# Kernel optimization log

Hardware: AMD Instinct MI355X
Metric: run time of the kernel (lower is better)

Reference implementation:

```python
import jax, jax.numpy as jnp
import numpy as np

N = 100000      # nodes
R = 4           # relations
E = 500000      # edges per relation
IN, HID, OUT = 256, 128, 64


def _graphconv(x, src, dst, W, b, n_nodes):
    """DGL GraphConv, norm='both': D_dst^{-1/2} A (D_src^{-1/2} x) W + b.
    Transform-first (in_feats >= out_feats path); math identical either way."""
    e = src.shape[0]
    ones = jnp.ones((e,), x.dtype)
    deg_out = jnp.clip(jax.ops.segment_sum(ones, src, num_segments=n_nodes), 1.0)
    deg_in = jnp.clip(jax.ops.segment_sum(ones, dst, num_segments=n_nodes), 1.0)
    h = (x * jax.lax.rsqrt(deg_out)[:, None]) @ W           # [N, out]
    agg = jax.ops.segment_sum(h[src], dst, num_segments=n_nodes)  # scatter-add over edges
    return agg * jax.lax.rsqrt(deg_in)[:, None] + b


def _hetero_layer(x, edges_src, edges_dst, W, b, n_nodes):
    # HeteroGraphConv(aggregate='sum'): sum of per-relation GraphConv outputs
    out = _graphconv(x, edges_src[0], edges_dst[0], W[0], b[0], n_nodes)
    for r in range(1, W.shape[0]):
        out = out + _graphconv(x, edges_src[r], edges_dst[r], W[r], b[r], n_nodes)
    return out


def setup_inputs() -> dict:
    key = jax.random.key(0)
    ks = jax.random.split(key, 8)
    x = jax.random.normal(ks[0], (N, IN), dtype=jnp.float32)
    edges_src = jax.random.randint(ks[1], (R, E), 0, N, dtype=jnp.int32)
    edges_dst = jax.random.randint(ks[2], (R, E), 0, N, dtype=jnp.int32)
    s1 = 1.0 / np.sqrt(IN)
    s2 = 1.0 / np.sqrt(HID)
    W1 = jax.random.uniform(ks[3], (R, IN, HID), jnp.float32, -s1, s1)
    b1 = jnp.zeros((R, HID), jnp.float32)
    W2 = jax.random.uniform(ks[4], (R, HID, OUT), jnp.float32, -s2, s2)
    b2 = jnp.zeros((R, OUT), jnp.float32)
    return {"x": x, "edges_src": edges_src, "edges_dst": edges_dst,
            "W1": W1, "b1": b1, "W2": W2, "b2": b2}


def reference(x, edges_src, edges_dst, W1, b1, W2, b2):
    h = _hetero_layer(x, edges_src, edges_dst, W1, b1, N)
    h = jax.nn.relu(h)
    out = _hetero_layer(h, edges_src, edges_dst, W2, b2, N)
    return out
```

## Files before the change

### kernel.cpp

```cpp
#include <hip/hip_runtime.h>

#define NN   100000
#define RR   4
#define EE   500000
#define FIN  256
#define FHID 128
#define FOUT 64
#define NBLK ((NN + 255) / 256)
#define NPAD (NN + 32)
#define NSHARD 8

#define PEDGE  ((RR * EE + 255) / 256)
#define PCW1   (RR * FIN * FHID / 256)
#define PCW2   (RR * FHID * FOUT / 256)
#define CONVW_GRID (PCW1 + PCW2 + 1)

#define NG1    ((NN + 127) / 128 * 4)
#define K1_PER 1564
#define K1_GRID (7 * K1_PER)

typedef unsigned short u16;
typedef unsigned char  u8;
typedef unsigned int   u32;
typedef __attribute__((ext_vector_type(8))) __bf16 bf16x8;
typedef __attribute__((ext_vector_type(4))) float  f32x4;
typedef __attribute__((ext_vector_type(4))) u32    u32x4;

__device__ __forceinline__ u16 f2bf(float f) {
    union { float f; u32 u; } v; v.f = f;
    u32 r = v.u + 0x7FFFu + ((v.u >> 16) & 1u);
    return (u16)(r >> 16);
}
__device__ __forceinline__ u32 pack2bf(float x, float y) {
    return ((u32)f2bf(y) << 16) | (u32)f2bf(x);
}

__device__ __forceinline__ float2 bfx2(u32 v) {
    union { u32 u; float f; } a, b;
    a.u = v << 16; b.u = v & 0xFFFF0000u;
    return {a.f, b.f};
}

typedef __attribute__((address_space(3))) u32 lds_u32;
typedef __attribute__((address_space(1))) const u32 gl_u32;
__device__ __forceinline__ void gload16(const void* g, void* l) {
    __builtin_amdgcn_global_load_lds((gl_u32*)g, (lds_u32*)l, 16, 0, 0);
}

__global__ __launch_bounds__(256) void convw_kernel(
        const float* __restrict__ W1, u16* __restrict__ W1t,
        const float* __restrict__ W2, u16* __restrict__ W2t,
        const float* __restrict__ b1, const float* __restrict__ b2,
        float* __restrict__ sb1, float* __restrict__ sb2) {
    int bx = blockIdx.x, t = threadIdx.x;
    if (bx < PCW1) {
        int i = bx * 256 + t;
        int r = i / (FIN * FHID);
        int rem = i - r * FIN * FHID;
        int k = rem / FHID, n = rem - k * FHID;
        W1t[((size_t)r * FHID + n) * FIN + k] = f2bf(W1[i]);
    } else if (bx < PCW1 + PCW2) {
        int i = (bx - PCW1) * 256 + t;
        int r = i / (FHID * FOUT);
        int rem = i - r * FHID * FOUT;
        int k = rem / FOUT, n = rem - k * FOUT;
        W2t[((size_t)r * FOUT + n) * FHID + k] = f2bf(W2[i]);
    } else {
        if (t < FHID) {
            float v = 0.f;
            for (int r = 0; r < RR; ++r) v += b1[r * FHID + t];
            sb1[t] = v;
        } else if (t < FHID + FOUT) {
            int j = t - FHID;
            float v = 0.f;
            for (int r = 0; r < RR; ++r) v += b2[r * FOUT + j];
            sb2[j] = v;
        }
    }
}

__device__ __forceinline__ void gemm1_body(u16* As, u16* Bs,
                                           const float* __restrict__ X,
                                           const u16* __restrict__ Bt,
                                           u16* __restrict__ Y, int M,
                                           int m0, int n0) {
    int tid = threadIdx.x;
    int wave = tid >> 6, lane = tid & 63;
    int quad = lane >> 4, l15 = lane & 15;
    int wm = (wave >> 1) * 64, wn = (wave & 1) * 64;

    int arow = tid >> 1;
    int acol = (tid & 1) * 16;
    const float4* Ag = (const float4*)(X + (size_t)min(m0 + arow, M - 1) * FIN + acol);
    u32* Aw = (u32*)As + arow * 16 + (acol >> 1);

    int srow = tid >> 2;
    int scol = (tid & 3) * 8;
    const u16* Bg0 = Bt + (size_t)(n0 + srow) * FIN + scol;
    const u16* Bg1 = Bt + (size_t)(n0 + srow + 64) * FIN + scol;
    u16* Bs0 = Bs + tid * 8;
    u16* Bs1 = Bs + 2048 + tid * 8;

    const bf16x8* Ard = (const bf16x8*)(As + (wm + l15) * 32 + quad * 8);
    const bf16x8* Brd = (const bf16x8*)(Bs + (wn + l15) * 32 + quad * 8);

    f32x4 acc[4][4] = {};
    for (int k0 = 0; k0 < FIN; k0 += 32) {
        gload16(Bg0 + k0, Bs0);
        gload16(Bg1 + k0, Bs1);
        float4 f0 = Ag[(k0 >> 2) + 0], f1 = Ag[(k0 >> 2) + 1];
        float4 f2 = Ag[(k0 >> 2) + 2], f3 = Ag[(k0 >> 2) + 3];
        u32x4 w0 = {pack2bf(f0.x, f0.y), pack2bf(f0.z, f0.w),
                    pack2bf(f1.x, f1.y), pack2bf(f1.z, f1.w)};
        u32x4 w1 = {pack2bf(f2.x, f2.y), pack2bf(f2.z, f2.w),
                    pack2bf(f3.x, f3.y), pack2bf(f3.z, f3.w)};
        ((u32x4*)Aw)[0] = w0;
        ((u32x4*)Aw)[1] = w1;
        __syncthreads();
        bf16x8 af[4], bfr[4];
#pragma unroll
        for (int i = 0; i < 4; ++i) af[i]  = Ard[i * 64];
#pragma unroll
        for (int j = 0; j < 4; ++j) bfr[j] = Brd[j * 64];
#pragma unroll
        for (int i = 0; i < 4; ++i)
#pragma unroll
            for (int j = 0; j < 4; ++j)
                acc[i][j] = __builtin_amdgcn_mfma_f32_16x16x32_bf16(af[i], bfr[j], acc[i][j], 0, 0, 0);
        __syncthreads();
    }

#pragma unroll
    for (int i = 0; i < 4; ++i) {
#pragma unroll
        for (int r = 0; r < 4; ++r) {
            int row = m0 + wm + i * 16 + quad * 4 + r;
            if (row < M) {
#pragma unroll
                for (int j = 0; j < 4; ++j) {
                    int col = n0 + wn + j * 16 + l15;
                    Y[(size_t)row * (RR * FHID) + col] = f2bf(acc[i][j][r]);
                }
            }
        }
    }
}

__global__ __launch_bounds__(256) void count_gemm(
        const float* __restrict__ x, const u16* __restrict__ W1t,
        u16* __restrict__ Y,
        const int* __restrict__ esrc, const int* __restrict__ edst,
        u32* __restrict__ cnt2,
        u8* __restrict__ pos8) {
    __shared__ u16 As[128 * 32];
    __shared__ u16 Bs[128 * 32];
    int p = blockIdx.x / 7, q = blockIdx.x - p * 7;
    if (q < 2) {
        int gb = p * 2 + q;
        if (gb >= NG1) return;
        gemm1_body(As, Bs, x, W1t, Y, NN, (gb >> 2) * 128, (gb & 3) * 128);
    } else {
        int i = (p * 5 + (q - 2)) * 256 + threadIdx.x;
        if (i >= RR * EE) return;
        u32* co = cnt2 + (size_t)(blockIdx.x & (NSHARD - 1)) * 2 * NPAD;
        int r = i / EE;
        int s = esrc[i], d = edst[i];
        atomicAdd(&co[s], 1u << (8 * r));
        u32 old = atomicAdd(&co[NPAD + d], 1u << (8 * r));
        pos8[i] = (u8)((old >> (8 * r)) & 255u);
    }
}

__global__ __launch_bounds__(256) void reduce_deg(const u32* __restrict__ cnt2,
                                                  f32x4* __restrict__ so,
                                                  f32x4* __restrict__ si,
                                                  u32x4* __restrict__ di4,
                                                  int* __restrict__ cnt,
                                                  int* __restrict__ bsum,
                                                  u8* __restrict__ shpre) {
    __shared__ int sh[256];
    int n = blockIdx.x * 256 + threadIdx.x;
    int c = 0;
    if (n < NN) {
        u32 osum[4] = {0, 0, 0, 0};
        u32 isum[4] = {0, 0, 0, 0};
        u32 words[8] = {0, 0, 0, 0, 0, 0, 0, 0};
#pragma unroll
        for (int s = 0; s < NSHARD; ++s) {
            u32 o = cnt2[(size_t)s * 2 * NPAD + n];
            u32 d = cnt2[(size_t)s * 2 * NPAD + NPAD + n];
#pragma unroll
            for (int k = 0; k < 4; ++k) {
                osum[k] += (o >> (8 * k)) & 255u;
                words[k * 2 + (s >> 2)] |= isum[k] << (8 * (s & 3));
                isum[k] += (d >> (8 * k)) & 255u;
            }
        }
        u32x4 dd;
        f32x4 vo, vi;
#pragma unroll
        for (int k = 0; k < 4; ++k) {
            dd[k] = isum[k];
            vo[k] = rsqrtf((float)max(osum[k], 1u));
            vi[k] = rsqrtf((float)max(isum[k], 1u));
            c += (int)isum[k];
        }
        so[n] = vo; si[n] = vi; di4[n] = dd;
        cnt[n] = c;
        u32x4* sp = (u32x4*)(shpre + (size_t)n * 32);
        u32x4 w0 = {words[0], words[1], words[2], words[3]};
        u32x4 w1 = {words[4], words[5], words[6], words[7]};
        sp[0] = w0;
        sp[1] = w1;
    }
    sh[threadIdx.x] = c;
    __syncthreads();
    for (int d = 128; d > 0; d >>= 1) {
        if (threadIdx.x < d) sh[threadIdx.x] += sh[threadIdx.x + d];
        __syncthreads();
    }
    if (threadIdx.x == 0) bsum[blockIdx.x] = sh[0];
}

__global__ __launch_bounds__(512) void scanb_kernel(const int* __restrict__ bsum,
                                                    int* __restrict__ boff) {
    __shared__ int sh[512];
    int t = threadIdx.x;
    int v = (t < NBLK) ? bsum[t] : 0;
    sh[t] = v;
    __syncthreads();
    for (int d = 1; d < 512; d <<= 1) {
        int u = (t >= d) ? sh[t - d] : 0;
        __syncthreads();
        sh[t] += u;
        __syncthreads();
    }
    if (t < NBLK) boff[t] = sh[t] - v;
}

__global__ __launch_bounds__(256) void offsets_kernel(const int* __restrict__ cnt,
                                                      const int* __restrict__ boff,
                                                      const u32x4* __restrict__ di4,
                                                      int* __restrict__ off,
                                                      u32x4* __restrict__ off4) {
    __shared__ int sh[256];
    int i = blockIdx.x * 256 + threadIdx.x;
    int t = threadIdx.x;
    int v = (i < NN) ? cnt[i] : 0;
    sh[t] = v;
    __syncthreads();
    for (int d = 1; d < 256; d <<= 1) {
        int u = (t >= d) ? sh[t - d] : 0;
        __syncthreads();
        sh[t] += u;
        __syncthreads();
    }
    int ex = boff[blockIdx.x] + sh[t] - v;
    if (i < NN) {
        off[i] = ex;
        u32x4 d = di4[i];
        u32x4 c;
        c[0] = (u32)ex;
        c[1] = c[0] + d[0];
        c[2] = c[1] + d[1];
        c[3] = c[2] + d[2];
        off4[i] = c;
    }
    if (i == NN - 1) off[NN] = ex + v;
}

__global__ __launch_bounds__(256) void place_kernel(const int* __restrict__ esrc,
                                                    const int* __restrict__ edst,
                                                    const u32* __restrict__ off4,
                                                    const u8* __restrict__ shpre,
                                                    const u8* __restrict__ pos8,
                                                    u32* __restrict__ meta) {
    int i = blockIdx.x * 256 + threadIdx.x;
    if (i >= RR * EE) return;
    int r = i / EE;
    int t = i >> 8;
    int p5 = t / 5;
    int shard = (p5 * 7 + (t - p5 * 5) + 2) & (NSHARD - 1);
    int dr = edst[i] * 4 + r;
    meta[off4[dr] + shpre[(size_t)dr * 8 + shard] + pos8[i]] = (u32)(esrc[i] * 4 + r);
}

template<int NW, int K, int LOG2F>
__global__ __launch_bounds__(256) void gemm_tile(const u16* __restrict__ A,
                                                 const u16* __restrict__ Bt,
                                                 const f32x4* __restrict__ so,
                                                 u16* __restrict__ Y, int M) {
    __shared__ u16 As[128 * 32];
    __shared__ u16 Bs[128 * 32];
    int tid = threadIdx.x;
    int m0 = blockIdx.x * 128, n0 = blockIdx.y * 128;
    int wave = tid >> 6, lane = tid & 63;
    int quad = lane >> 4, l15 = lane & 15;
    int wm = (wave >> 1) * 64, wn = (wave & 1) * 64;

    int srow = tid >> 2;
    int scol = (tid & 3) * 8;
    const u16* Ag0 = A + (size_t)min(m0 + srow,      M - 1) * K + scol;
    const u16* Ag1 = A + (size_t)min(m0 + srow + 64, M - 1) * K + scol;
    const u16* Bg0 = Bt + (size_t)(n0 + srow) * K + scol;
    const u16* Bg1 = Bt + (size_t)(n0 + srow + 64) * K + scol;
    u16* As0 = As + tid * 8;
    u16* As1 = As + 2048 + tid * 8;
    u16* Bs0 = Bs + tid * 8;
    u16* Bs1 = Bs + 2048 + tid * 8;

    const bf16x8* Ard = (const bf16x8*)(As + (wm + l15) * 32 + quad * 8);
    const bf16x8* Brd = (const bf16x8*)(Bs + (wn + l15) * 32 + quad * 8);

    f32x4 acc[4][4] = {};
    for (int k0 = 0; k0 < K; k0 += 32) {
        gload16(Ag0 + k0, As0);
        gload16(Ag1 + k0, As1);
        gload16(Bg0 + k0, Bs0);
        gload16(Bg1 + k0, Bs1);
        __syncthreads();
        bf16x8 af[4], bfr[4];
#pragma unroll
        for (int i = 0; i < 4; ++i) af[i]  = Ard[i * 64];
#pragma unroll
        for (int j = 0; j < 4; ++j) bfr[j] = Brd[j * 64];
#pragma unroll
        for (int i = 0; i < 4; ++i)
#pragma unroll
            for (int j = 0; j < 4; ++j)
                acc[i][j] = __builtin_amdgcn_mfma_f32_16x16x32_bf16(af[i], bfr[j], acc[i][j], 0, 0, 0);
        __syncthreads();
    }

#pragma unroll
    for (int i = 0; i < 4; ++i) {
#pragma unroll
        for (int r = 0; r < 4; ++r) {
            int row = m0 + wm + i * 16 + quad * 4 + r;
            if (row < M) {
                f32x4 so4 = so[row];
#pragma unroll
                for (int j = 0; j < 4; ++j) {
                    int colb = n0 + wn + j * 16;
                    float scale = so4[colb >> LOG2F];
                    Y[(size_t)row * NW + colb + l15] = f2bf(acc[i][j][r] * scale);
                }
            }
        }
    }
}


__global__ __launch_bounds__(256) void gather1(const u32* __restrict__ Y,
                                               const int* __restrict__ off,
                                               const u32* __restrict__ meta,
                                               const float* __restrict__ soF,
                                               const f32x4* __restrict__ si,
                                               const float* __restrict__ sb,
                                               u32* __restrict__ H1) {
    int wid  = blockIdx.x * 4 + (threadIdx.x >> 6);
    int lane = threadIdx.x & 63;
    if (wid >= NN) return;
    int j = off[wid], end = off[wid + 1];
    f32x4 si4 = si[wid];
    float a0x = 0.f, a0y = 0.f, a1x = 0.f, a1y = 0.f;
    float a2x = 0.f, a2y = 0.f, a3x = 0.f, a3y = 0.f;
    for (; j + 4 <= end; j += 4) {
        u32 m0 = meta[j], m1 = meta[j + 1], m2 = meta[j + 2], m3 = meta[j + 3];
        u32 v0 = Y[(size_t)m0 * 64 + lane];
        u32 v1 = Y[(size_t)m1 * 64 + lane];
        u32 v2 = Y[(size_t)m2 * 64 + lane];
        u32 v3 = Y[(size_t)m3 * 64 + lane];
        float c0 = soF[m0] * si4[m0 & 3], c1 = soF[m1] * si4[m1 & 3];
        float c2 = soF[m2] * si4[m2 & 3], c3 = soF[m3] * si4[m3 & 3];
        float2 f0 = bfx2(v0), f1 = bfx2(v1), f2 = bfx2(v2), f3 = bfx2(v3);
        a0x = fmaf(c0, f0.x, a0x); a0y = fmaf(c0, f0.y, a0y);
        a1x = fmaf(c1, f1.x, a1x); a1y = fmaf(c1, f1.y, a1y);
        a2x = fmaf(c2, f2.x, a2x); a2y = fmaf(c2, f2.y, a2y);
        a3x = fmaf(c3, f3.x, a3x); a3y = fmaf(c3, f3.y, a3y);
    }
    for (; j < end; ++j) {
        u32 m0 = meta[j];
        u32 v0 = Y[(size_t)m0 * 64 + lane];
        float2 f0 = bfx2(v0);
        float c0 = soF[m0] * si4[m0 & 3];
        a0x = fmaf(c0, f0.x, a0x); a0y = fmaf(c0, f0.y, a0y);
    }
    float2 b = ((const float2*)sb)[lane];
    float ax = fmaxf((a0x + a1x) + (a2x + a3x) + b.x, 0.f);
    float ay = fmaxf((a0y + a1y) + (a2y + a3y) + b.y, 0.f);
    H1[(size_t)wid * 64 + lane] = ((u32)f2bf(ay) << 16) | (u32)f2bf(ax);
}

__global__ __launch_bounds__(256) void gather2(const u32* __restrict__ Y,
                                               const int* __restrict__ off,
                                               const u32* __restrict__ meta,
                                               const f32x4* __restrict__ si,
                                               const float* __restrict__ sb,
                                               float* __restrict__ out) {
    int wid  = blockIdx.x * 4 + (threadIdx.x >> 6);
    int lane = threadIdx.x & 63;
    if (wid >= NN) return;
    int sub = lane >> 5, col = lane & 31;
    int end = off[wid + 1];
    int j = off[wid] + sub;
    f32x4 si4 = si[wid];
    float a0x = 0.f, a0y = 0.f, a1x = 0.f, a1y = 0.f;
    for (; j + 2 < end; j += 4) {
        u32 m0 = meta[j], m1 = meta[j + 2];
        u32 v0 = Y[(size_t)m0 * 32 + col];
        u32 v1 = Y[(size_t)m1 * 32 + col];
        float2 f0 = bfx2(v0), f1 = bfx2(v1);
        float c0 = si4[m0 & 3], c1 = si4[m1 & 3];
        a0x = fmaf(c0, f0.x, a0x); a0y = fmaf(c0, f0.y, a0y);
        a1x = fmaf(c1, f1.x, a1x); a1y = fmaf(c1, f1.y, a1y);
    }
    if (j < end) {
        u32 m0 = meta[j];
        u32 v0 = Y[(size_t)m0 * 32 + col];
        float2 f0 = bfx2(v0);
        float c0 = si4[m0 & 3];
        a0x = fmaf(c0, f0.x, a0x); a0y = fmaf(c0, f0.y, a0y);
    }
    float ax = a0x + a1x, ay = a0y + a1y;
    ax += __shfl_xor(ax, 32);
    ay += __shfl_xor(ay, 32);
    if (sub == 0) {
        float2 b = ((const float2*)sb)[col];
        float2 o = {ax + b.x, ay + b.y};
        ((float2*)out)[(size_t)wid * 32 + col] = o;
    }
}


extern "C" void kernel_launch(void* const* d_in, const int* in_sizes, int n_in,
                              void* d_out, int out_size, void* d_ws, size_t ws_size,
                              hipStream_t stream) {
    const float* x    = (const float*)d_in[0];
    const int*   esrc = (const int*)  d_in[1];
    const int*   edst = (const int*)  d_in[2];
    const float* W1   = (const float*)d_in[3];
    const float* b1   = (const float*)d_in[4];
    const float* W2   = (const float*)d_in[5];
    const float* b2   = (const float*)d_in[6];
    float* out = (float*)d_out;

    char* w = (char*)d_ws;
    auto alloc = [&](size_t bytes) -> char* {
        char* p = w; w += (bytes + 255) & ~(size_t)255; return p;
    };
    u32*   cnt2    = (u32*)  alloc((size_t)NSHARD * 2 * NPAD * 4);
    float* so      = (float*)alloc((size_t)NN * 4 * 4);
    float* si      = (float*)alloc((size_t)NN * 4 * 4);
    u32*   di4     = (u32*)  alloc((size_t)NN * 4 * 4);
    int*   cnt     = (int*)  alloc((size_t)NN * 4);
    int*   off     = (int*)  alloc((size_t)(NN + 1) * 4);
    u32*   off4    = (u32*)  alloc((size_t)NN * 4 * 4);
    int*   bsum    = (int*)  alloc((size_t)NBLK * 4);
    int*   boff    = (int*)  alloc((size_t)NBLK * 4);
    float* sb1     = (float*)alloc(FHID * 4);
    float* sb2     = (float*)alloc(FOUT * 4);
    u8*    shpre   = (u8*)   alloc((size_t)NN * 4 * NSHARD);
    u8*    pos8    = (u8*)   alloc((size_t)RR * EE);
    u16*   W1t     = (u16*)  alloc((size_t)RR * FIN * FHID * 2);
    u16*   W2t     = (u16*)  alloc((size_t)RR * FHID * FOUT * 2);
    u32*   meta    = (u32*)  alloc((size_t)RR * EE * 4);
    u16*   H1bf    = (u16*)  alloc((size_t)NN * FHID * 2);
    u16*   Yall    = (u16*)  alloc((size_t)NN * RR * FHID * 2);

    hipMemsetAsync(cnt2, 0, (size_t)NSHARD * 2 * NPAD * 4, stream);

    convw_kernel<<<CONVW_GRID, 256, 0, stream>>>(W1, W1t, W2, W2t, b1, b2, sb1, sb2);

    count_gemm<<<K1_GRID, 256, 0, stream>>>(x, W1t, Yall, esrc, edst, cnt2, pos8);

    reduce_deg<<<NBLK, 256, 0, stream>>>(cnt2, (f32x4*)so, (f32x4*)si,
                                         (u32x4*)di4, cnt, bsum, shpre);
    scanb_kernel<<<1, 512, 0, stream>>>(bsum, boff);
    offsets_kernel<<<NBLK, 256, 0, stream>>>(cnt, boff, (const u32x4*)di4, off, (u32x4*)off4);
    place_kernel<<<PEDGE, 256, 0, stream>>>(esrc, edst, off4, shpre, pos8, meta);

    gather1<<<(NN + 3) / 4, 256, 0, stream>>>((const u32*)Yall, off, meta,
                                              so, (const f32x4*)si, sb1, (u32*)H1bf);

    {
        dim3 grid((NN + 127) / 128, (RR * FOUT) / 128);
        gemm_tile<RR * FOUT, FHID, 6><<<grid, 256, 0, stream>>>(H1bf, W2t, (const f32x4*)so, Yall, NN);
    }
    gather2<<<(NN + 3) / 4, 256, 0, stream>>>((const u32*)Yall, off, meta,
                                              (const f32x4*)si, sb2, out);
}
```

Before: 585.8 us.

## Replace sharded degree counters with single global counters and batch edge atomics

```diff
diff --git a/kernel.cpp b/kernel.cpp
--- a/kernel.cpp
+++ b/kernel.cpp
@@ -8,7 +8,6 @@
 #define FOUT 64
 #define NBLK ((NN + 255) / 256)
 #define NPAD (NN + 32)
-#define NSHARD 8
 
 #define PEDGE  ((RR * EE + 255) / 256)
 #define PCW1   (RR * FIN * FHID / 256)
@@ -18,6 +17,7 @@
 #define NG1    ((NN + 127) / 128 * 4)
 #define K1_PER 1564
 #define K1_GRID (7 * K1_PER)
+#define CEDGE  ((RR * EE + 1023) / 1024)
 
 typedef unsigned short u16;
 typedef unsigned char  u8;
@@ -150,7 +150,7 @@
         const float* __restrict__ x, const u16* __restrict__ W1t,
         u16* __restrict__ Y,
         const int* __restrict__ esrc, const int* __restrict__ edst,
-        u32* __restrict__ cnt2,
+        u32* __restrict__ counto, u32* __restrict__ counti,
         u8* __restrict__ pos8) {
     __shared__ u16 As[128 * 32];
     __shared__ u16 Bs[128 * 32];
@@ -160,58 +160,66 @@
         if (gb >= NG1) return;
         gemm1_body(As, Bs, x, W1t, Y, NN, (gb >> 2) * 128, (gb & 3) * 128);
     } else {
-        int i = (p * 5 + (q - 2)) * 256 + threadIdx.x;
-        if (i >= RR * EE) return;
-        u32* co = cnt2 + (size_t)(blockIdx.x & (NSHARD - 1)) * 2 * NPAD;
-        int r = i / EE;
-        int s = esrc[i], d = edst[i];
-        atomicAdd(&co[s], 1u << (8 * r));
-        u32 old = atomicAdd(&co[NPAD + d], 1u << (8 * r));
-        pos8[i] = (u8)((old >> (8 * r)) & 255u);
-    }
-}
-
-__global__ __launch_bounds__(256) void reduce_deg(const u32* __restrict__ cnt2,
+        int cb = p * 5 + (q - 2);
+        if (cb >= CEDGE) return;
+        int i0 = cb * 1024 + threadIdx.x;
+        if (cb < CEDGE - 1) {
+            int rr[4], dd[4];
+            u32 olds[4];
+#pragma unroll
+            for (int k = 0; k < 4; ++k) {
+                int i = i0 + k * 256;
+                int r = i / EE;
+                rr[k] = r;
+                int s = esrc[i];
+                dd[k] = edst[i];
+                atomicAdd(&counto[s], 1u << (8 * r));
+            }
+#pragma unroll
+            for (int k = 0; k < 4; ++k)
+                olds[k] = atomicAdd(&counti[dd[k]], 1u << (8 * rr[k]));
+#pragma unroll
+            for (int k = 0; k < 4; ++k)
+                pos8[i0 + k * 256] = (u8)((olds[k] >> (8 * rr[k])) & 255u);
+        } else {
+            for (int k = 0; k < 4; ++k) {
+                int i = i0 + k * 256;
+                if (i >= RR * EE) break;
+                int r = i / EE;
+                int s = esrc[i], d = edst[i];
+                atomicAdd(&counto[s], 1u << (8 * r));
+                u32 old = atomicAdd(&counti[d], 1u << (8 * r));
+                pos8[i] = (u8)((old >> (8 * r)) & 255u);
+            }
+        }
+    }
+}
+
+__global__ __launch_bounds__(256) void reduce_deg(const u32* __restrict__ counto,
+                                                  const u32* __restrict__ counti,
                                                   f32x4* __restrict__ so,
                                                   f32x4* __restrict__ si,
                                                   u32x4* __restrict__ di4,
                                                   int* __restrict__ cnt,
-                                                  int* __restrict__ bsum,
-                                                  u8* __restrict__ shpre) {
+                                                  int* __restrict__ bsum) {
     __shared__ int sh[256];
     int n = blockIdx.x * 256 + threadIdx.x;
     int c = 0;
     if (n < NN) {
-        u32 osum[4] = {0, 0, 0, 0};
-        u32 isum[4] = {0, 0, 0, 0};
-        u32 words[8] = {0, 0, 0, 0, 0, 0, 0, 0};
-#pragma unroll
-        for (int s = 0; s < NSHARD; ++s) {
-            u32 o = cnt2[(size_t)s * 2 * NPAD + n];
-            u32 d = cnt2[(size_t)s * 2 * NPAD + NPAD + n];
-#pragma unroll
-            for (int k = 0; k < 4; ++k) {
-                osum[k] += (o >> (8 * k)) & 255u;
-                words[k * 2 + (s >> 2)] |= isum[k] << (8 * (s & 3));
-                isum[k] += (d >> (8 * k)) & 255u;
-            }
-        }
+        u32 o = counto[n], d = counti[n];
         u32x4 dd;
         f32x4 vo, vi;
 #pragma unroll
         for (int k = 0; k < 4; ++k) {
-            dd[k] = isum[k];
-            vo[k] = rsqrtf((float)max(osum[k], 1u));
-            vi[k] = rsqrtf((float)max(isum[k], 1u));
-            c += (int)isum[k];
+            u32 ob = (o >> (8 * k)) & 255u;
+            u32 db = (d >> (8 * k)) & 255u;
+            dd[k] = db;
+            vo[k] = rsqrtf((float)max(ob, 1u));
+            vi[k] = rsqrtf((float)max(db, 1u));
+            c += (int)db;
         }
         so[n] = vo; si[n] = vi; di4[n] = dd;
         cnt[n] = c;
-        u32x4* sp = (u32x4*)(shpre + (size_t)n * 32);
-        u32x4 w0 = {words[0], words[1], words[2], words[3]};
-        u32x4 w1 = {words[4], words[5], words[6], words[7]};
-        sp[0] = w0;
-        sp[1] = w1;
     }
     sh[threadIdx.x] = c;
     __syncthreads();
@@ -272,17 +280,12 @@
 __global__ __launch_bounds__(256) void place_kernel(const int* __restrict__ esrc,
                                                     const int* __restrict__ edst,
                                                     const u32* __restrict__ off4,
-                                                    const u8* __restrict__ shpre,
                                                     const u8* __restrict__ pos8,
                                                     u32* __restrict__ meta) {
     int i = blockIdx.x * 256 + threadIdx.x;
     if (i >= RR * EE) return;
     int r = i / EE;
-    int t = i >> 8;
-    int p5 = t / 5;
-    int shard = (p5 * 7 + (t - p5 * 5) + 2) & (NSHARD - 1);
-    int dr = edst[i] * 4 + r;
-    meta[off4[dr] + shpre[(size_t)dr * 8 + shard] + pos8[i]] = (u32)(esrc[i] * 4 + r);
+    meta[off4[edst[i] * 4 + r] + pos8[i]] = (u32)(esrc[i] * 4 + r);
 }
 
 template<int NW, int K, int LOG2F>
@@ -449,7 +452,9 @@
     auto alloc = [&](size_t bytes) -> char* {
         char* p = w; w += (bytes + 255) & ~(size_t)255; return p;
     };
-    u32*   cnt2    = (u32*)  alloc((size_t)NSHARD * 2 * NPAD * 4);
+    u32*   cnt2    = (u32*)  alloc((size_t)2 * NPAD * 4);
+    u32*   counto  = cnt2;
+    u32*   counti  = cnt2 + NPAD;
     float* so      = (float*)alloc((size_t)NN * 4 * 4);
     float* si      = (float*)alloc((size_t)NN * 4 * 4);
     u32*   di4     = (u32*)  alloc((size_t)NN * 4 * 4);
@@ -460,7 +465,6 @@
     int*   boff    = (int*)  alloc((size_t)NBLK * 4);
     float* sb1     = (float*)alloc(FHID * 4);
     float* sb2     = (float*)alloc(FOUT * 4);
-    u8*    shpre   = (u8*)   alloc((size_t)NN * 4 * NSHARD);
     u8*    pos8    = (u8*)   alloc((size_t)RR * EE);
     u16*   W1t     = (u16*)  alloc((size_t)RR * FIN * FHID * 2);
     u16*   W2t     = (u16*)  alloc((size_t)RR * FHID * FOUT * 2);
@@ -468,17 +472,18 @@
     u16*   H1bf    = (u16*)  alloc((size_t)NN * FHID * 2);
     u16*   Yall    = (u16*)  alloc((size_t)NN * RR * FHID * 2);
 
-    hipMemsetAsync(cnt2, 0, (size_t)NSHARD * 2 * NPAD * 4, stream);
+    hipMemsetAsync(cnt2, 0, (size_t)2 * NPAD * 4, stream);
 
     convw_kernel<<<CONVW_GRID, 256, 0, stream>>>(W1, W1t, W2, W2t, b1, b2, sb1, sb2);
 
-    count_gemm<<<K1_GRID, 256, 0, stream>>>(x, W1t, Yall, esrc, edst, cnt2, pos8);
-
-    reduce_deg<<<NBLK, 256, 0, stream>>>(cnt2, (f32x4*)so, (f32x4*)si,
-                                         (u32x4*)di4, cnt, bsum, shpre);
+    count_gemm<<<K1_GRID, 256, 0, stream>>>(x, W1t, Yall, esrc, edst,
+                                            counto, counti, pos8);
+
+    reduce_deg<<<NBLK, 256, 0, stream>>>(counto, counti,
+                                         (f32x4*)so, (f32x4*)si, (u32x4*)di4, cnt, bsum);
     scanb_kernel<<<1, 512, 0, stream>>>(bsum, boff);
     offsets_kernel<<<NBLK, 256, 0, stream>>>(cnt, boff, (const u32x4*)di4, off, (u32x4*)off4);
-    place_kernel<<<PEDGE, 256, 0, stream>>>(esrc, edst, off4, shpre, pos8, meta);
+    place_kernel<<<PEDGE, 256, 0, stream>>>(esrc, edst, off4, pos8, meta);
 
     gather1<<<(NN + 3) / 4, 256, 0, stream>>>((const u32*)Yall, off, meta,
                                               so, (const f32x4*)si, sb1, (u32*)H1bf);
```

New measurement: 592.5 us. No clear change (+1.1%).
